# Kernel optimization log

Measured on AMD Instinct MI355X. Metric: run time of the kernel, lower is better.

Reference implementation:

```python
import jax, jax.numpy as jnp
import numpy as np

N_NODES = 100000
N_EDGES = 2000000
D_IN = 4
HID = 64


def setup_inputs() -> dict:
    key = jax.random.key(0)
    ks = jax.random.split(key, 8)
    node_feats = jax.random.normal(ks[0], (N_NODES, D_IN), dtype=jnp.float32)
    pairs = jax.random.randint(ks[1], (N_EDGES, 2), 0, N_NODES, dtype=jnp.int64)
    # Kaiming-ish init scaling
    W1 = jax.random.normal(ks[2], (D_IN, HID), dtype=jnp.float32) / np.sqrt(D_IN)
    b1 = jnp.zeros((HID,), dtype=jnp.float32)
    W2 = jax.random.normal(ks[3], (HID, HID), dtype=jnp.float32) / np.sqrt(HID)
    b2 = jnp.zeros((HID,), dtype=jnp.float32)
    We1 = jax.random.normal(ks[4], (3 * HID, HID), dtype=jnp.float32) / np.sqrt(3 * HID)
    be1 = jnp.zeros((HID,), dtype=jnp.float32)
    We2 = jax.random.normal(ks[5], (HID, 1), dtype=jnp.float32) / np.sqrt(HID)
    be2 = jnp.zeros((1,), dtype=jnp.float32)
    return {"node_feats": node_feats, "pairs": pairs, "W1": W1, "b1": b1,
            "W2": W2, "b2": b2, "We1": We1, "be1": be1, "We2": We2, "be2": be2}


def reference(node_feats, pairs, W1, b1, W2, b2, We1, be1, We2, be2):
    # node MLP: Linear -> ReLU -> Linear -> ReLU
    H = jax.nn.relu(node_feats @ W1 + b1)      # [N, HID]
    H = jax.nn.relu(H @ W2 + b2)               # [N, HID]
    # vectorized gather over all edge pairs (replaces Python loop)
    hu = H[pairs[:, 0]]                        # [E, HID]
    hv = H[pairs[:, 1]]                        # [E, HID]
    E = jnp.concatenate([hu, hv, jnp.abs(hu - hv)], axis=-1)  # [E, 3*HID]
    # edge MLP: Linear -> ReLU -> Linear, squeeze last dim
    scores = (jax.nn.relu(E @ We1 + be1) @ We2 + be2)[:, 0]   # [E]
    return scores
```

## Files before the change

### kernel.cpp

```cpp
#include <hip/hip_runtime.h>

#define N_NODES 100000
#define N_EDGES 2000000

typedef __bf16 bf16x8 __attribute__((ext_vector_type(8)));
typedef float f32x4 __attribute__((ext_vector_type(4)));
typedef float f32x16 __attribute__((ext_vector_type(16)));

__device__ __forceinline__ unsigned f2bf_rne(float f) {
  unsigned u = __builtin_bit_cast(unsigned, f);
  u += 0x7FFFu + ((u >> 16) & 1u);
  return u >> 16;
}

__device__ __forceinline__ unsigned pack_rhu(float lo, float hi) {
  unsigned ulo = __builtin_bit_cast(unsigned, lo) + 0x8000u;
  unsigned uhi = __builtin_bit_cast(unsigned, hi) + 0x8000u;
  return __builtin_amdgcn_perm(uhi, ulo, 0x07060302u);
}

__device__ __forceinline__ unsigned absdiff_pack(unsigned a, unsigned b) {
  float alo = __builtin_bit_cast(float, a << 16);
  float ahi = __builtin_bit_cast(float, a & 0xFFFF0000u);
  float blo = __builtin_bit_cast(float, b << 16);
  float bhi = __builtin_bit_cast(float, b & 0xFFFF0000u);
  return pack_rhu(fabsf(alo - blo), fabsf(ahi - bhi));
}

__global__ __launch_bounds__(64, 1) void node_mfma_kernel(
    const float* __restrict__ X, const float* __restrict__ W1,
    const float* __restrict__ b1, const float* __restrict__ W2,
    const float* __restrict__ b2, unsigned short* __restrict__ H) {
  const int lane = threadIdx.x;
  const int l15 = lane & 15;
  const int quad = lane >> 4;

  float w1v[2][4][8], b1v[2][8];
#pragma unroll
  for (int c = 0; c < 2; ++c)
#pragma unroll
    for (int j = 0; j < 8; ++j) {
      int col = c * 32 + quad * 8 + j;
      b1v[c][j] = b1[col];
#pragma unroll
      for (int d = 0; d < 4; ++d) w1v[c][d][j] = W1[d * 64 + col];
    }

  uint4 afr[2][4];
#pragma unroll
  for (int c = 0; c < 2; ++c)
#pragma unroll
    for (int mt = 0; mt < 4; ++mt) {
      unsigned w[4];
#pragma unroll
      for (int p = 0; p < 4; ++p) {
        int k = c * 32 + quad * 8 + 2 * p;
        unsigned lo = f2bf_rne(W2[k * 64 + mt * 16 + l15]);
        unsigned hi = f2bf_rne(W2[(k + 1) * 64 + mt * 16 + l15]);
        w[p] = lo | (hi << 16);
      }
      afr[c][mt] = make_uint4(w[0], w[1], w[2], w[3]);
    }
  float b2v[16];
#pragma unroll
  for (int mt = 0; mt < 4; ++mt)
#pragma unroll
    for (int r = 0; r < 4; ++r) b2v[mt * 4 + r] = b2[mt * 16 + quad * 4 + r];

  const int ntiles = N_NODES / 16;
  for (int tile = blockIdx.x; tile < ntiles; tile += gridDim.x) {
    float4 xv = ((const float4*)X)[tile * 16 + l15];

    uint4 bfr[2];
#pragma unroll
    for (int c = 0; c < 2; ++c) {
      unsigned w[4];
#pragma unroll
      for (int p = 0; p < 4; ++p) {
        float h0 = fmaxf(b1v[c][2 * p] + xv.x * w1v[c][0][2 * p] +
                             xv.y * w1v[c][1][2 * p] + xv.z * w1v[c][2][2 * p] +
                             xv.w * w1v[c][3][2 * p],
                         0.f);
        float h1 = fmaxf(b1v[c][2 * p + 1] + xv.x * w1v[c][0][2 * p + 1] +
                             xv.y * w1v[c][1][2 * p + 1] +
                             xv.z * w1v[c][2][2 * p + 1] +
                             xv.w * w1v[c][3][2 * p + 1],
                         0.f);
        w[p] = pack_rhu(h0, h1);
      }
      bfr[c] = make_uint4(w[0], w[1], w[2], w[3]);
    }

    f32x4 acc[4];
#pragma unroll
    for (int mt = 0; mt < 4; ++mt) acc[mt] = (f32x4){0.f, 0.f, 0.f, 0.f};
#pragma unroll
    for (int c = 0; c < 2; ++c)
#pragma unroll
      for (int mt = 0; mt < 4; ++mt)
        acc[mt] = __builtin_amdgcn_mfma_f32_16x16x32_bf16(
            __builtin_bit_cast(bf16x8, afr[c][mt]),
            __builtin_bit_cast(bf16x8, bfr[c]), acc[mt], 0, 0, 0);

    unsigned short* hrow = H + (tile * 16 + l15) * 64;
#pragma unroll
    for (int mt = 0; mt < 4; ++mt) {
      unsigned lo = pack_rhu(fmaxf(acc[mt][0] + b2v[mt * 4 + 0], 0.f),
                             fmaxf(acc[mt][1] + b2v[mt * 4 + 1], 0.f));
      unsigned hi = pack_rhu(fmaxf(acc[mt][2] + b2v[mt * 4 + 2], 0.f),
                             fmaxf(acc[mt][3] + b2v[mt * 4 + 3], 0.f));
      *(uint2*)(hrow + mt * 16 + quad * 4) = make_uint2(lo, hi);
    }
  }
}

__global__ __launch_bounds__(256, 2) void edge_mlp_kernel(
    const unsigned short* __restrict__ H, const int* __restrict__ pairs,
    const float* __restrict__ We1, const float* __restrict__ be1,
    const float* __restrict__ We2, const float* __restrict__ be2,
    float* __restrict__ out) {
  const int tid = threadIdx.x;
  const int lane = tid & 63;
  const int n = lane & 31;
  const int half = lane >> 5;
  const int wave = tid >> 6;

  uint4 afr[13][2];
#pragma unroll
  for (int c = 0; c < 12; ++c)
#pragma unroll
    for (int mt = 0; mt < 2; ++mt) {
      int col = mt * 32 + n;
      int kb = c * 16 + half * 8;
      unsigned w[4];
#pragma unroll
      for (int p = 0; p < 4; ++p)
        w[p] = f2bf_rne(We1[(kb + 2 * p) * 64 + col]) |
               (f2bf_rne(We1[(kb + 2 * p + 1) * 64 + col]) << 16);
      afr[c][mt] = make_uint4(w[0], w[1], w[2], w[3]);
    }
#pragma unroll
  for (int mt = 0; mt < 2; ++mt)
    afr[12][mt] =
        make_uint4((half == 0) ? f2bf_rne(be1[mt * 32 + n]) : 0u, 0u, 0u, 0u);

  const uint4 b13u = make_uint4((half == 0) ? 0x00003F80u : 0u, 0u, 0u, 0u);

  float we2v[32];
#pragma unroll
  for (int mt = 0; mt < 2; ++mt)
#pragma unroll
    for (int r = 0; r < 16; ++r)
      we2v[mt * 16 + r] = We2[mt * 32 + (r & 3) + 8 * (r >> 2) + 4 * half];
  const float be2v = be2[0];

  const int wid = blockIdx.x * 4 + wave;
  const int nw = gridDim.x * 4;
  const int ntiles = N_EDGES / 32;
  const int last = ntiles - 1;
  const int2* pairs2 = (const int2*)pairs;

  const unsigned short* Hh = H + half * 8;

  int2 pr = pairs2[(size_t)wid * 32 + n];
  uint4 hu[4], hv[4];
  {
    const uint4* pu = (const uint4*)(Hh + (size_t)pr.x * 64);
    const uint4* pv = (const uint4*)(Hh + (size_t)pr.y * 64);
#pragma unroll
    for (int c = 0; c < 4; ++c) {
      hu[c] = pu[2 * c];
      hv[c] = pv[2 * c];
    }
  }
  {
    int t1 = wid + nw;
    if (t1 > last) t1 = last;
    pr = pairs2[(size_t)t1 * 32 + n];
  }

  for (int t = wid; t < ntiles; t += nw) {
    uint4 ab[4];
#pragma unroll
    for (int c = 0; c < 4; ++c) {
      ab[c].x = absdiff_pack(hu[c].x, hv[c].x);
      ab[c].y = absdiff_pack(hu[c].y, hv[c].y);
      ab[c].z = absdiff_pack(hu[c].z, hv[c].z);
      ab[c].w = absdiff_pack(hu[c].w, hv[c].w);
    }

    f32x16 acc[2];
    acc[0] = (f32x16)(0.f);
    acc[1] = (f32x16)(0.f);

#pragma unroll
    for (int c = 0; c < 4; ++c) {
      bf16x8 b = __builtin_bit_cast(bf16x8, hu[c]);
#pragma unroll
      for (int mt = 0; mt < 2; ++mt)
        acc[mt] = __builtin_amdgcn_mfma_f32_32x32x16_bf16(
            __builtin_bit_cast(bf16x8, afr[c][mt]), b, acc[mt], 0, 0, 0);
    }
#pragma unroll
    for (int c = 0; c < 4; ++c) {
      bf16x8 b = __builtin_bit_cast(bf16x8, hv[c]);
#pragma unroll
      for (int mt = 0; mt < 2; ++mt)
        acc[mt] = __builtin_amdgcn_mfma_f32_32x32x16_bf16(
            __builtin_bit_cast(bf16x8, afr[4 + c][mt]), b, acc[mt], 0, 0, 0);
    }

    {
      const uint4* pu = (const uint4*)(Hh + (size_t)pr.x * 64);
      const uint4* pv = (const uint4*)(Hh + (size_t)pr.y * 64);
#pragma unroll
      for (int c = 0; c < 4; ++c) {
        hu[c] = pu[2 * c];
        hv[c] = pv[2 * c];
      }
      int t2 = t + 2 * nw;
      if (t2 > last) t2 = last;
      pr = pairs2[(size_t)t2 * 32 + n];
    }
    __builtin_amdgcn_sched_barrier(0);

#pragma unroll
    for (int c = 0; c < 4; ++c) {
      bf16x8 b = __builtin_bit_cast(bf16x8, ab[c]);
#pragma unroll
      for (int mt = 0; mt < 2; ++mt)
        acc[mt] = __builtin_amdgcn_mfma_f32_32x32x16_bf16(
            __builtin_bit_cast(bf16x8, afr[8 + c][mt]), b, acc[mt], 0, 0, 0);
    }
#pragma unroll
    for (int mt = 0; mt < 2; ++mt)
      acc[mt] = __builtin_amdgcn_mfma_f32_32x32x16_bf16(
          __builtin_bit_cast(bf16x8, afr[12][mt]),
          __builtin_bit_cast(bf16x8, b13u), acc[mt], 0, 0, 0);

    float s = 0.f;
#pragma unroll
    for (int mt = 0; mt < 2; ++mt)
#pragma unroll
      for (int r = 0; r < 16; ++r)
        s += fmaxf(acc[mt][r], 0.f) * we2v[mt * 16 + r];
    s += __shfl_xor(s, 32);
    if (half == 0) out[t * 32 + n] = s + be2v;
  }
}

extern "C" void kernel_launch(void* const* d_in, const int* in_sizes, int n_in,
                              void* d_out, int out_size, void* d_ws,
                              size_t ws_size, hipStream_t stream) {
  const float* X = (const float*)d_in[0];
  const int* pairs = (const int*)d_in[1];
  const float* W1 = (const float*)d_in[2];
  const float* b1 = (const float*)d_in[3];
  const float* W2 = (const float*)d_in[4];
  const float* b2 = (const float*)d_in[5];
  const float* We1 = (const float*)d_in[6];
  const float* be1 = (const float*)d_in[7];
  const float* We2 = (const float*)d_in[8];
  const float* be2 = (const float*)d_in[9];
  float* out = (float*)d_out;
  unsigned short* H = (unsigned short*)d_ws;

  node_mfma_kernel<<<1024, 64, 0, stream>>>(X, W1, b1, W2, b2, H);
  edge_mlp_kernel<<<512, 256, 0, stream>>>(H, pairs, We1, be1, We2, be2, out);
}
```

Before: 175.0 us.

## Stage edge-MLP weights in LDS, fold bias into epilogue, raise occupancy

The We1 bf16 fragments move from per-thread registers into a shared LDS array that the four waves fill cooperatively. Each MFMA now reads its A operand from LDS. The bias is no longer applied by an extra MFMA on a constant-one column; it is added in the ReLU epilogue from registers. The lower register pressure allows launch bounds of 3 blocks per SIMD and a 768-block grid, trading LDS read traffic on every MFMA for more waves to hide the latency of the random gathers.

```diff
diff --git a/kernel.cpp b/kernel.cpp
--- a/kernel.cpp
+++ b/kernel.cpp
@@ -114,44 +114,45 @@
   }
 }
 
-__global__ __launch_bounds__(256, 2) void edge_mlp_kernel(
+__global__ __launch_bounds__(256, 3) void edge_mlp_kernel(
     const unsigned short* __restrict__ H, const int* __restrict__ pairs,
     const float* __restrict__ We1, const float* __restrict__ be1,
     const float* __restrict__ We2, const float* __restrict__ be2,
     float* __restrict__ out) {
+  __shared__ uint4 lds_w[12][2][64];
+
   const int tid = threadIdx.x;
   const int lane = tid & 63;
   const int n = lane & 31;
   const int half = lane >> 5;
   const int wave = tid >> 6;
 
-  uint4 afr[13][2];
-#pragma unroll
-  for (int c = 0; c < 12; ++c)
+#pragma unroll
+  for (int ci = 0; ci < 3; ++ci) {
+    const int c = wave * 3 + ci;
 #pragma unroll
     for (int mt = 0; mt < 2; ++mt) {
-      int col = mt * 32 + n;
-      int kb = c * 16 + half * 8;
+      const int col = mt * 32 + n;
+      const int kb = c * 16 + half * 8;
       unsigned w[4];
 #pragma unroll
       for (int p = 0; p < 4; ++p)
         w[p] = f2bf_rne(We1[(kb + 2 * p) * 64 + col]) |
                (f2bf_rne(We1[(kb + 2 * p + 1) * 64 + col]) << 16);
-      afr[c][mt] = make_uint4(w[0], w[1], w[2], w[3]);
-    }
+      lds_w[c][mt][lane] = make_uint4(w[0], w[1], w[2], w[3]);
+    }
+  }
+  __syncthreads();
+
+  float we2v[32], be1v[32];
 #pragma unroll
   for (int mt = 0; mt < 2; ++mt)
-    afr[12][mt] =
-        make_uint4((half == 0) ? f2bf_rne(be1[mt * 32 + n]) : 0u, 0u, 0u, 0u);
-
-  const uint4 b13u = make_uint4((half == 0) ? 0x00003F80u : 0u, 0u, 0u, 0u);
-
-  float we2v[32];
-#pragma unroll
-  for (int mt = 0; mt < 2; ++mt)
-#pragma unroll
-    for (int r = 0; r < 16; ++r)
-      we2v[mt * 16 + r] = We2[mt * 32 + (r & 3) + 8 * (r >> 2) + 4 * half];
+#pragma unroll
+    for (int r = 0; r < 16; ++r) {
+      const int o = mt * 32 + (r & 3) + 8 * (r >> 2) + 4 * half;
+      we2v[mt * 16 + r] = We2[o];
+      be1v[mt * 16 + r] = be1[o];
+    }
   const float be2v = be2[0];
 
   const int wid = blockIdx.x * 4 + wave;
@@ -195,19 +196,23 @@
 
 #pragma unroll
     for (int c = 0; c < 4; ++c) {
-      bf16x8 b = __builtin_bit_cast(bf16x8, hu[c]);
-#pragma unroll
-      for (int mt = 0; mt < 2; ++mt)
-        acc[mt] = __builtin_amdgcn_mfma_f32_32x32x16_bf16(
-            __builtin_bit_cast(bf16x8, afr[c][mt]), b, acc[mt], 0, 0, 0);
-    }
-#pragma unroll
-    for (int c = 0; c < 4; ++c) {
-      bf16x8 b = __builtin_bit_cast(bf16x8, hv[c]);
-#pragma unroll
-      for (int mt = 0; mt < 2; ++mt)
-        acc[mt] = __builtin_amdgcn_mfma_f32_32x32x16_bf16(
-            __builtin_bit_cast(bf16x8, afr[4 + c][mt]), b, acc[mt], 0, 0, 0);
+      const bf16x8 b = __builtin_bit_cast(bf16x8, hu[c]);
+      const uint4 a0 = lds_w[c][0][lane];
+      const uint4 a1 = lds_w[c][1][lane];
+      acc[0] = __builtin_amdgcn_mfma_f32_32x32x16_bf16(
+          __builtin_bit_cast(bf16x8, a0), b, acc[0], 0, 0, 0);
+      acc[1] = __builtin_amdgcn_mfma_f32_32x32x16_bf16(
+          __builtin_bit_cast(bf16x8, a1), b, acc[1], 0, 0, 0);
+    }
+#pragma unroll
+    for (int c = 0; c < 4; ++c) {
+      const bf16x8 b = __builtin_bit_cast(bf16x8, hv[c]);
+      const uint4 a0 = lds_w[4 + c][0][lane];
+      const uint4 a1 = lds_w[4 + c][1][lane];
+      acc[0] = __builtin_amdgcn_mfma_f32_32x32x16_bf16(
+          __builtin_bit_cast(bf16x8, a0), b, acc[0], 0, 0, 0);
+      acc[1] = __builtin_amdgcn_mfma_f32_32x32x16_bf16(
+          __builtin_bit_cast(bf16x8, a1), b, acc[1], 0, 0, 0);
     }
 
     {
@@ -226,24 +231,21 @@
 
 #pragma unroll
     for (int c = 0; c < 4; ++c) {
-      bf16x8 b = __builtin_bit_cast(bf16x8, ab[c]);
-#pragma unroll
-      for (int mt = 0; mt < 2; ++mt)
-        acc[mt] = __builtin_amdgcn_mfma_f32_32x32x16_bf16(
-            __builtin_bit_cast(bf16x8, afr[8 + c][mt]), b, acc[mt], 0, 0, 0);
-    }
+      const bf16x8 b = __builtin_bit_cast(bf16x8, ab[c]);
+      const uint4 a0 = lds_w[8 + c][0][lane];
+      const uint4 a1 = lds_w[8 + c][1][lane];
+      acc[0] = __builtin_amdgcn_mfma_f32_32x32x16_bf16(
+          __builtin_bit_cast(bf16x8, a0), b, acc[0], 0, 0, 0);
+      acc[1] = __builtin_amdgcn_mfma_f32_32x32x16_bf16(
+          __builtin_bit_cast(bf16x8, a1), b, acc[1], 0, 0, 0);
+    }
+
+    float s = 0.f;
 #pragma unroll
     for (int mt = 0; mt < 2; ++mt)
-      acc[mt] = __builtin_amdgcn_mfma_f32_32x32x16_bf16(
-          __builtin_bit_cast(bf16x8, afr[12][mt]),
-          __builtin_bit_cast(bf16x8, b13u), acc[mt], 0, 0, 0);
-
-    float s = 0.f;
-#pragma unroll
-    for (int mt = 0; mt < 2; ++mt)
 #pragma unroll
       for (int r = 0; r < 16; ++r)
-        s += fmaxf(acc[mt][r], 0.f) * we2v[mt * 16 + r];
+        s += fmaxf(acc[mt][r] + be1v[mt * 16 + r], 0.f) * we2v[mt * 16 + r];
     s += __shfl_xor(s, 32);
     if (half == 0) out[t * 32 + n] = s + be2v;
   }
@@ -266,5 +268,5 @@
   unsigned short* H = (unsigned short*)d_ws;
 
   node_mfma_kernel<<<1024, 64, 0, stream>>>(X, W1, b1, W2, b2, H);
-  edge_mlp_kernel<<<512, 256, 0, stream>>>(H, pairs, We1, be1, We2, be2, out);
-}
+  edge_mlp_kernel<<<768, 256, 0, stream>>>(H, pairs, We1, be1, We2, be2, out);
+}
```

Result: slower. 201.5 us (+15.1%).
